# Performance work log

Hardware: AMD Instinct MI355X
Metric: run time of the kernel (lower is better)

The kernel has to match this reference:

```python
import jax, jax.numpy as jnp
import numpy as np

H = 128  # hidden_size
I = 28   # input_size
C = 10   # num_classes


def setup_inputs() -> dict:
    key = jax.random.key(0)
    ks = jax.random.split(key, 11)
    s = 1.0 / np.sqrt(H)  # torch nn.RNN init scale
    return {
        "x": jax.random.normal(ks[0], (8192, 28, I), dtype=jnp.float32),
        "W_ih0": jax.random.uniform(ks[1], (H, I), jnp.float32, -s, s),
        "W_hh0": jax.random.uniform(ks[2], (H, H), jnp.float32, -s, s),
        "b_ih0": jax.random.uniform(ks[3], (H,), jnp.float32, -s, s),
        "b_hh0": jax.random.uniform(ks[4], (H,), jnp.float32, -s, s),
        "W_ih1": jax.random.uniform(ks[5], (H, H), jnp.float32, -s, s),
        "W_hh1": jax.random.uniform(ks[6], (H, H), jnp.float32, -s, s),
        "b_ih1": jax.random.uniform(ks[7], (H,), jnp.float32, -s, s),
        "b_hh1": jax.random.uniform(ks[8], (H,), jnp.float32, -s, s),
        "fc_w": jax.random.uniform(ks[9], (C, H), jnp.float32, -s, s),
        "fc_b": jax.random.uniform(ks[10], (C,), jnp.float32, -s, s),
    }


def _rnn_layer_full(x, W_ih, b_ih, W_hh, b_hh):
    # x: [B, T, D] -> full output sequence [B, T, H]
    B = x.shape[0]
    h0 = jnp.zeros((B, H), x.dtype)
    xw = jnp.einsum('btd,hd->bth', x, W_ih) + b_ih  # precompute input GEMM

    def step(h, xw_t):
        h = jnp.tanh(xw_t + h @ W_hh.T + b_hh)
        return h, h

    _, ys = jax.lax.scan(step, h0, jnp.swapaxes(xw, 0, 1))  # [T, B, H]
    return jnp.swapaxes(ys, 0, 1)


def _rnn_layer_last(x, W_ih, b_ih, W_hh, b_hh):
    # only the final hidden state is needed downstream
    B = x.shape[0]
    h0 = jnp.zeros((B, H), x.dtype)
    xw = jnp.einsum('btd,hd->bth', x, W_ih) + b_ih

    def step(h, xw_t):
        h = jnp.tanh(xw_t + h @ W_hh.T + b_hh)
        return h, None

    h_last, _ = jax.lax.scan(step, h0, jnp.swapaxes(xw, 0, 1))
    return h_last


def reference(x, W_ih0, W_hh0, b_ih0, b_hh0, W_ih1, W_hh1, b_ih1, b_hh1, fc_w, fc_b):
    out0 = _rnn_layer_full(x, W_ih0, b_ih0, W_hh0, b_hh0)   # [B, T, H]
    h_last = _rnn_layer_last(out0, W_ih1, b_ih1, W_hh1, b_hh1)  # [B, H] == out[:, -1, :]
    return h_last @ fc_w.T + fc_b  # [B, C]
```

## Files before the change

kernel.cpp:

```cpp
#include <hip/hip_runtime.h>
#include <cmath>

#define HSZ 128
#define ISZ 28
#define TSZ 28
#define CSZ 10
#define BT  16
#define NT  256
#define HP  136

typedef _Float16 half_t;
typedef _Float16 v8h __attribute__((ext_vector_type(8)));
typedef float v4f __attribute__((ext_vector_type(4)));

__device__ __forceinline__ float fast_tanh(float x) {
    x = fminf(fmaxf(x, -15.f), 15.f);
    float e = __expf(2.f * x);
    return (e - 1.f) * __builtin_amdgcn_rcpf(e + 1.f);
}

__global__ __launch_bounds__(NT, 2)
void rnn_mfma(const float* __restrict__ x,
              const float* __restrict__ W_ih0, const float* __restrict__ W_hh0,
              const float* __restrict__ b_ih0, const float* __restrict__ b_hh0,
              const float* __restrict__ W_ih1, const float* __restrict__ W_hh1,
              const float* __restrict__ b_ih1, const float* __restrict__ b_hh1,
              const float* __restrict__ fc_w, const float* __restrict__ fc_b,
              float* __restrict__ out)
{
    __shared__ half_t h0s[2][BT][HP];
    __shared__ half_t h1s[2][BT][HP];
    __shared__ half_t xss[2][BT][32];

    const int tid  = threadIdx.x;
    const int wave = tid >> 6;
    const int lane = tid & 63;
    const int ln   = lane & 15;
    const int quad = lane >> 4;
    const int kq   = quad * 8;
    const int b0   = blockIdx.x * BT;

    v8h bWx[2];
    v8h bW0[2][4];
    v8h bW1i[2][4];
    v8h bW1h[2][4];
    float bias0v[2], bias1v[2];

#pragma unroll
    for (int nj = 0; nj < 2; ++nj) {
        const int c = (wave * 2 + nj) * 16 + ln;
        bias0v[nj] = b_ih0[c] + b_hh0[c];
        bias1v[nj] = b_ih1[c] + b_hh1[c];
#pragma unroll
        for (int j = 0; j < 8; ++j) {
            const int k = kq + j;
            bWx[nj][j] = (half_t)(k < ISZ ? W_ih0[c * ISZ + k] : 0.f);
        }
#pragma unroll
        for (int ks = 0; ks < 4; ++ks) {
            const float* p0 = W_hh0 + c * HSZ + ks * 32 + kq;
            const float* p1 = W_ih1 + c * HSZ + ks * 32 + kq;
            const float* p2 = W_hh1 + c * HSZ + ks * 32 + kq;
#pragma unroll
            for (int j = 0; j < 8; ++j) {
                bW0[nj][ks][j]  = (half_t)p0[j];
                bW1i[nj][ks][j] = (half_t)p1[j];
                bW1h[nj][ks][j] = (half_t)p2[j];
            }
        }
    }

    for (int idx = tid; idx < BT * HP; idx += NT) {
        (&h0s[0][0][0])[idx] = (half_t)0.f;
        (&h1s[0][0][0])[idx] = (half_t)0.f;
    }
    for (int idx = tid; idx < BT * 32; idx += NT) {
        const int m = idx >> 5, i = idx & 31;
        xss[0][m][i] = (half_t)(i < ISZ ? x[(size_t)(b0 + m) * (TSZ * ISZ) + i] : 0.f);
    }
    __syncthreads();

    int cA = 0, cB = 0;
    for (int t = 0; t < TSZ; ++t) {
        const int tb = t & 1;

        if (t + 1 < TSZ) {
            for (int idx = tid; idx < BT * 32; idx += NT) {
                const int m = idx >> 5, i = idx & 31;
                xss[tb ^ 1][m][i] =
                    (half_t)(i < ISZ ? x[(size_t)(b0 + m) * (TSZ * ISZ) + (t + 1) * ISZ + i]
                                     : 0.f);
            }
        }

        v4f acc[2];
#pragma unroll
        for (int nj = 0; nj < 2; ++nj)
            acc[nj] = (v4f){bias0v[nj], bias0v[nj], bias0v[nj], bias0v[nj]};
        {
            const v8h ax = *(const v8h*)&xss[tb][ln][kq];
#pragma unroll
            for (int nj = 0; nj < 2; ++nj)
                acc[nj] = __builtin_amdgcn_mfma_f32_16x16x32_f16(ax, bWx[nj], acc[nj], 0, 0, 0);
        }
#pragma unroll
        for (int ks = 0; ks < 4; ++ks) {
            const v8h ah = *(const v8h*)&h0s[cA][ln][ks * 32 + kq];
#pragma unroll
            for (int nj = 0; nj < 2; ++nj)
                acc[nj] = __builtin_amdgcn_mfma_f32_16x16x32_f16(ah, bW0[nj][ks], acc[nj], 0, 0, 0);
        }
#pragma unroll
        for (int nj = 0; nj < 2; ++nj) {
            const int c = (wave * 2 + nj) * 16 + ln;
#pragma unroll
            for (int r = 0; r < 4; ++r)
                h0s[cA ^ 1][quad * 4 + r][c] = (half_t)fast_tanh(acc[nj][r]);
        }
        __syncthreads();

#pragma unroll
        for (int nj = 0; nj < 2; ++nj)
            acc[nj] = (v4f){bias1v[nj], bias1v[nj], bias1v[nj], bias1v[nj]};
#pragma unroll
        for (int ks = 0; ks < 4; ++ks) {
            const v8h a0 = *(const v8h*)&h0s[cA ^ 1][ln][ks * 32 + kq];
#pragma unroll
            for (int nj = 0; nj < 2; ++nj)
                acc[nj] = __builtin_amdgcn_mfma_f32_16x16x32_f16(a0, bW1i[nj][ks], acc[nj], 0, 0, 0);
            const v8h a1 = *(const v8h*)&h1s[cB][ln][ks * 32 + kq];
#pragma unroll
            for (int nj = 0; nj < 2; ++nj)
                acc[nj] = __builtin_amdgcn_mfma_f32_16x16x32_f16(a1, bW1h[nj][ks], acc[nj], 0, 0, 0);
        }
#pragma unroll
        for (int nj = 0; nj < 2; ++nj) {
            const int c = (wave * 2 + nj) * 16 + ln;
#pragma unroll
            for (int r = 0; r < 4; ++r)
                h1s[cB ^ 1][quad * 4 + r][c] = (half_t)fast_tanh(acc[nj][r]);
        }
        __syncthreads();
        cA ^= 1; cB ^= 1;
    }

    for (int idx = tid; idx < BT * CSZ; idx += NT) {
        const int m = idx / CSZ, cc = idx - m * CSZ;
        float s = fc_b[cc];
#pragma unroll 4
        for (int k = 0; k < HSZ; ++k)
            s += (float)h1s[cB][m][k] * fc_w[cc * HSZ + k];
        out[(b0 + m) * CSZ + cc] = s;
    }
}

extern "C" void kernel_launch(void* const* d_in, const int* in_sizes, int n_in,
                              void* d_out, int out_size, void* d_ws, size_t ws_size,
                              hipStream_t stream) {
    const float* x     = (const float*)d_in[0];
    const float* W_ih0 = (const float*)d_in[1];
    const float* W_hh0 = (const float*)d_in[2];
    const float* b_ih0 = (const float*)d_in[3];
    const float* b_hh0 = (const float*)d_in[4];
    const float* W_ih1 = (const float*)d_in[5];
    const float* W_hh1 = (const float*)d_in[6];
    const float* b_ih1 = (const float*)d_in[7];
    const float* b_hh1 = (const float*)d_in[8];
    const float* fc_w  = (const float*)d_in[9];
    const float* fc_b  = (const float*)d_in[10];
    float* out = (float*)d_out;

    const int B = in_sizes[0] / (TSZ * ISZ);
    dim3 grid(B / BT), block(NT);
    rnn_mfma<<<grid, block, 0, stream>>>(x, W_ih0, W_hh0, b_ih0, b_hh0,
                                         W_ih1, W_hh1, b_ih1, b_hh1,
                                         fc_w, fc_b, out);
}
```

Measured before the change: 148.0 us.

## Skew layer-1 one step behind layer-0 to merge both recurrences per sync

Layer 1 now runs one timestep behind layer 0, so each iteration computes layer-0 step t+1 and layer-1 step t from the same loaded hidden states, with one barrier per step instead of two. The MFMA operands are swapped so weights are the A operand and hidden states the B operand, which lets tanh outputs be stored as packed 4-half vectors. The change also simplifies tanh by dropping the clamp, vectorizes the weight loads and the final FC, and adds a prologue and epilogue step. The cost is more live registers and a slightly more complex schedule; removing the clamp relies on exp overflow behaving well.

```diff
diff --git a/kernel.cpp b/kernel.cpp
--- a/kernel.cpp
+++ b/kernel.cpp
@@ -1,5 +1,4 @@
 #include <hip/hip_runtime.h>
-#include <cmath>
 
 #define HSZ 128
 #define ISZ 28
@@ -8,29 +7,30 @@
 #define BT  16
 #define NT  256
 #define HP  136
+#define XP  40
 
 typedef _Float16 half_t;
 typedef _Float16 v8h __attribute__((ext_vector_type(8)));
+typedef _Float16 v4h __attribute__((ext_vector_type(4)));
 typedef float v4f __attribute__((ext_vector_type(4)));
 
 __device__ __forceinline__ float fast_tanh(float x) {
-    x = fminf(fmaxf(x, -15.f), 15.f);
     float e = __expf(2.f * x);
-    return (e - 1.f) * __builtin_amdgcn_rcpf(e + 1.f);
+    return 1.f - 2.f * __builtin_amdgcn_rcpf(e + 1.f);
 }
 
 __global__ __launch_bounds__(NT, 2)
-void rnn_mfma(const float* __restrict__ x,
-              const float* __restrict__ W_ih0, const float* __restrict__ W_hh0,
-              const float* __restrict__ b_ih0, const float* __restrict__ b_hh0,
-              const float* __restrict__ W_ih1, const float* __restrict__ W_hh1,
-              const float* __restrict__ b_ih1, const float* __restrict__ b_hh1,
-              const float* __restrict__ fc_w, const float* __restrict__ fc_b,
-              float* __restrict__ out)
+void rnn_mfma2(const float* __restrict__ x,
+               const float* __restrict__ W_ih0, const float* __restrict__ W_hh0,
+               const float* __restrict__ b_ih0, const float* __restrict__ b_hh0,
+               const float* __restrict__ W_ih1, const float* __restrict__ W_hh1,
+               const float* __restrict__ b_ih1, const float* __restrict__ b_hh1,
+               const float* __restrict__ fc_w, const float* __restrict__ fc_b,
+               float* __restrict__ out)
 {
-    __shared__ half_t h0s[2][BT][HP];
-    __shared__ half_t h1s[2][BT][HP];
-    __shared__ half_t xss[2][BT][32];
+    __shared__ half_t h0s[2][BT * HP];
+    __shared__ half_t h1s[2][BT * HP];
+    __shared__ half_t xss[2][BT * XP];
 
     const int tid  = threadIdx.x;
     const int wave = tid >> 6;
@@ -40,116 +40,162 @@
     const int kq   = quad * 8;
     const int b0   = blockIdx.x * BT;
 
-    v8h bWx[2];
-    v8h bW0[2][4];
-    v8h bW1i[2][4];
-    v8h bW1h[2][4];
-    float bias0v[2], bias1v[2];
-
-#pragma unroll
-    for (int nj = 0; nj < 2; ++nj) {
-        const int c = (wave * 2 + nj) * 16 + ln;
-        bias0v[nj] = b_ih0[c] + b_hh0[c];
-        bias1v[nj] = b_ih1[c] + b_hh1[c];
+    v8h aWx[2];
+    v8h aW0[2][4];
+    v8h aW1i[2][4];
+    v8h aW1h[2][4];
+    v4f bias0[2], bias1[2];
+
+#pragma unroll
+    for (int nt = 0; nt < 2; ++nt) {
+        const int base = (wave * 2 + nt) * 16;
+        const int row  = base + ln;
+#pragma unroll
+        for (int r = 0; r < 4; ++r) {
+            const int c = base + quad * 4 + r;
+            bias0[nt][r] = b_ih0[c] + b_hh0[c];
+            bias1[nt][r] = b_ih1[c] + b_hh1[c];
+        }
 #pragma unroll
         for (int j = 0; j < 8; ++j) {
             const int k = kq + j;
-            bWx[nj][j] = (half_t)(k < ISZ ? W_ih0[c * ISZ + k] : 0.f);
-        }
-#pragma unroll
-        for (int ks = 0; ks < 4; ++ks) {
-            const float* p0 = W_hh0 + c * HSZ + ks * 32 + kq;
-            const float* p1 = W_ih1 + c * HSZ + ks * 32 + kq;
-            const float* p2 = W_hh1 + c * HSZ + ks * 32 + kq;
-#pragma unroll
-            for (int j = 0; j < 8; ++j) {
-                bW0[nj][ks][j]  = (half_t)p0[j];
-                bW1i[nj][ks][j] = (half_t)p1[j];
-                bW1h[nj][ks][j] = (half_t)p2[j];
+            aWx[nt][j] = (half_t)(k < ISZ ? W_ih0[row * ISZ + k] : 0.f);
+        }
+#pragma unroll
+        for (int ks = 0; ks < 4; ++ks) {
+            const float4* p0 = (const float4*)(W_hh0 + row * HSZ + ks * 32 + kq);
+            const float4* p1 = (const float4*)(W_ih1 + row * HSZ + ks * 32 + kq);
+            const float4* p2 = (const float4*)(W_hh1 + row * HSZ + ks * 32 + kq);
+            float4 a = p0[0], b = p0[1];
+            aW0[nt][ks] = (v8h){(half_t)a.x, (half_t)a.y, (half_t)a.z, (half_t)a.w,
+                                (half_t)b.x, (half_t)b.y, (half_t)b.z, (half_t)b.w};
+            a = p1[0]; b = p1[1];
+            aW1i[nt][ks] = (v8h){(half_t)a.x, (half_t)a.y, (half_t)a.z, (half_t)a.w,
+                                 (half_t)b.x, (half_t)b.y, (half_t)b.z, (half_t)b.w};
+            a = p2[0]; b = p2[1];
+            aW1h[nt][ks] = (v8h){(half_t)a.x, (half_t)a.y, (half_t)a.z, (half_t)a.w,
+                                 (half_t)b.x, (half_t)b.y, (half_t)b.z, (half_t)b.w};
+        }
+    }
+
+    for (int idx = tid; idx < BT * XP; idx += NT) {
+        xss[0][idx] = (half_t)0.f;
+        xss[1][idx] = (half_t)0.f;
+    }
+    for (int idx = tid; idx < BT * HP; idx += NT)
+        h1s[0][idx] = (half_t)0.f;
+    __syncthreads();
+    for (int idx = tid; idx < BT * ISZ; idx += NT) {
+        const int m = idx / ISZ, i = idx - m * ISZ;
+        const float* xr = x + (size_t)(b0 + m) * (TSZ * ISZ);
+        xss[0][m * XP + i] = (half_t)xr[i];
+        xss[1][m * XP + i] = (half_t)(ISZ + i < 2 * ISZ ? xr[ISZ + i] : 0.f);
+    }
+    __syncthreads();
+
+    {
+        const v8h bx = *(const v8h*)&xss[0][ln * XP + kq];
+        v4f a0[2] = {bias0[0], bias0[1]};
+#pragma unroll
+        for (int nt = 0; nt < 2; ++nt)
+            a0[nt] = __builtin_amdgcn_mfma_f32_16x16x32_f16(aWx[nt], bx, a0[nt], 0, 0, 0);
+#pragma unroll
+        for (int nt = 0; nt < 2; ++nt) {
+            const int base = (wave * 2 + nt) * 16;
+            v4h p = {(half_t)fast_tanh(a0[nt][0]), (half_t)fast_tanh(a0[nt][1]),
+                     (half_t)fast_tanh(a0[nt][2]), (half_t)fast_tanh(a0[nt][3])};
+            *(v4h*)&h0s[0][ln * HP + base + quad * 4] = p;
+        }
+    }
+    __syncthreads();
+
+    for (int t = 0; t < TSZ - 1; ++t) {
+        const int pr = t & 1;
+
+        if (t < TSZ - 2) {
+            for (int idx = tid; idx < BT * ISZ; idx += NT) {
+                const int m = idx / ISZ, i = idx - m * ISZ;
+                xss[pr][m * XP + i] =
+                    (half_t)x[(size_t)(b0 + m) * (TSZ * ISZ) + (t + 2) * ISZ + i];
             }
         }
-    }
-
-    for (int idx = tid; idx < BT * HP; idx += NT) {
-        (&h0s[0][0][0])[idx] = (half_t)0.f;
-        (&h1s[0][0][0])[idx] = (half_t)0.f;
-    }
-    for (int idx = tid; idx < BT * 32; idx += NT) {
-        const int m = idx >> 5, i = idx & 31;
-        xss[0][m][i] = (half_t)(i < ISZ ? x[(size_t)(b0 + m) * (TSZ * ISZ) + i] : 0.f);
-    }
-    __syncthreads();
-
-    int cA = 0, cB = 0;
-    for (int t = 0; t < TSZ; ++t) {
-        const int tb = t & 1;
-
-        if (t + 1 < TSZ) {
-            for (int idx = tid; idx < BT * 32; idx += NT) {
-                const int m = idx >> 5, i = idx & 31;
-                xss[tb ^ 1][m][i] =
-                    (half_t)(i < ISZ ? x[(size_t)(b0 + m) * (TSZ * ISZ) + (t + 1) * ISZ + i]
-                                     : 0.f);
+
+        v8h bh0[4], bh1[4];
+#pragma unroll
+        for (int ks = 0; ks < 4; ++ks) {
+            bh0[ks] = *(const v8h*)&h0s[pr][ln * HP + ks * 32 + kq];
+            bh1[ks] = *(const v8h*)&h1s[pr][ln * HP + ks * 32 + kq];
+        }
+        const v8h bx = *(const v8h*)&xss[pr ^ 1][ln * XP + kq];
+
+        v4f a1[2] = {bias1[0], bias1[1]};
+        v4f a0[2] = {bias0[0], bias0[1]};
+#pragma unroll
+        for (int nt = 0; nt < 2; ++nt)
+            a0[nt] = __builtin_amdgcn_mfma_f32_16x16x32_f16(aWx[nt], bx, a0[nt], 0, 0, 0);
+#pragma unroll
+        for (int ks = 0; ks < 4; ++ks) {
+#pragma unroll
+            for (int nt = 0; nt < 2; ++nt) {
+                a1[nt] = __builtin_amdgcn_mfma_f32_16x16x32_f16(aW1i[nt][ks], bh0[ks], a1[nt], 0, 0, 0);
+                a1[nt] = __builtin_amdgcn_mfma_f32_16x16x32_f16(aW1h[nt][ks], bh1[ks], a1[nt], 0, 0, 0);
+                a0[nt] = __builtin_amdgcn_mfma_f32_16x16x32_f16(aW0[nt][ks], bh0[ks], a0[nt], 0, 0, 0);
             }
         }
 
-        v4f acc[2];
-#pragma unroll
-        for (int nj = 0; nj < 2; ++nj)
-            acc[nj] = (v4f){bias0v[nj], bias0v[nj], bias0v[nj], bias0v[nj]};
-        {
-            const v8h ax = *(const v8h*)&xss[tb][ln][kq];
-#pragma unroll
-            for (int nj = 0; nj < 2; ++nj)
-                acc[nj] = __builtin_amdgcn_mfma_f32_16x16x32_f16(ax, bWx[nj], acc[nj], 0, 0, 0);
-        }
-#pragma unroll
-        for (int ks = 0; ks < 4; ++ks) {
-            const v8h ah = *(const v8h*)&h0s[cA][ln][ks * 32 + kq];
-#pragma unroll
-            for (int nj = 0; nj < 2; ++nj)
-                acc[nj] = __builtin_amdgcn_mfma_f32_16x16x32_f16(ah, bW0[nj][ks], acc[nj], 0, 0, 0);
-        }
-#pragma unroll
-        for (int nj = 0; nj < 2; ++nj) {
-            const int c = (wave * 2 + nj) * 16 + ln;
-#pragma unroll
-            for (int r = 0; r < 4; ++r)
-                h0s[cA ^ 1][quad * 4 + r][c] = (half_t)fast_tanh(acc[nj][r]);
+#pragma unroll
+        for (int nt = 0; nt < 2; ++nt) {
+            const int base = (wave * 2 + nt) * 16;
+            v4h p1 = {(half_t)fast_tanh(a1[nt][0]), (half_t)fast_tanh(a1[nt][1]),
+                      (half_t)fast_tanh(a1[nt][2]), (half_t)fast_tanh(a1[nt][3])};
+            *(v4h*)&h1s[pr ^ 1][ln * HP + base + quad * 4] = p1;
+            v4h p0 = {(half_t)fast_tanh(a0[nt][0]), (half_t)fast_tanh(a0[nt][1]),
+                      (half_t)fast_tanh(a0[nt][2]), (half_t)fast_tanh(a0[nt][3])};
+            *(v4h*)&h0s[pr ^ 1][ln * HP + base + quad * 4] = p0;
         }
         __syncthreads();
-
-#pragma unroll
-        for (int nj = 0; nj < 2; ++nj)
-            acc[nj] = (v4f){bias1v[nj], bias1v[nj], bias1v[nj], bias1v[nj]};
-#pragma unroll
-        for (int ks = 0; ks < 4; ++ks) {
-            const v8h a0 = *(const v8h*)&h0s[cA ^ 1][ln][ks * 32 + kq];
-#pragma unroll
-            for (int nj = 0; nj < 2; ++nj)
-                acc[nj] = __builtin_amdgcn_mfma_f32_16x16x32_f16(a0, bW1i[nj][ks], acc[nj], 0, 0, 0);
-            const v8h a1 = *(const v8h*)&h1s[cB][ln][ks * 32 + kq];
-#pragma unroll
-            for (int nj = 0; nj < 2; ++nj)
-                acc[nj] = __builtin_amdgcn_mfma_f32_16x16x32_f16(a1, bW1h[nj][ks], acc[nj], 0, 0, 0);
-        }
-#pragma unroll
-        for (int nj = 0; nj < 2; ++nj) {
-            const int c = (wave * 2 + nj) * 16 + ln;
-#pragma unroll
-            for (int r = 0; r < 4; ++r)
-                h1s[cB ^ 1][quad * 4 + r][c] = (half_t)fast_tanh(acc[nj][r]);
+    }
+
+    {
+        const int pr = (TSZ - 1) & 1;
+        v8h bh0[4], bh1[4];
+#pragma unroll
+        for (int ks = 0; ks < 4; ++ks) {
+            bh0[ks] = *(const v8h*)&h0s[pr][ln * HP + ks * 32 + kq];
+            bh1[ks] = *(const v8h*)&h1s[pr][ln * HP + ks * 32 + kq];
+        }
+        v4f a1[2] = {bias1[0], bias1[1]};
+#pragma unroll
+        for (int ks = 0; ks < 4; ++ks) {
+#pragma unroll
+            for (int nt = 0; nt < 2; ++nt) {
+                a1[nt] = __builtin_amdgcn_mfma_f32_16x16x32_f16(aW1i[nt][ks], bh0[ks], a1[nt], 0, 0, 0);
+                a1[nt] = __builtin_amdgcn_mfma_f32_16x16x32_f16(aW1h[nt][ks], bh1[ks], a1[nt], 0, 0, 0);
+            }
+        }
+#pragma unroll
+        for (int nt = 0; nt < 2; ++nt) {
+            const int base = (wave * 2 + nt) * 16;
+            v4h p1 = {(half_t)fast_tanh(a1[nt][0]), (half_t)fast_tanh(a1[nt][1]),
+                      (half_t)fast_tanh(a1[nt][2]), (half_t)fast_tanh(a1[nt][3])};
+            *(v4h*)&h1s[pr ^ 1][ln * HP + base + quad * 4] = p1;
         }
         __syncthreads();
-        cA ^= 1; cB ^= 1;
-    }
-
-    for (int idx = tid; idx < BT * CSZ; idx += NT) {
-        const int m = idx / CSZ, cc = idx - m * CSZ;
+    }
+
+    if (tid < BT * CSZ) {
+        const int m = tid / CSZ, cc = tid - m * CSZ;
         float s = fc_b[cc];
-#pragma unroll 4
-        for (int k = 0; k < HSZ; ++k)
-            s += (float)h1s[cB][m][k] * fc_w[cc * HSZ + k];
+#pragma unroll
+        for (int k8 = 0; k8 < HSZ / 8; ++k8) {
+            const v8h hv = *(const v8h*)&h1s[0][m * HP + k8 * 8];
+            const float4 w0 = *(const float4*)(fc_w + cc * HSZ + k8 * 8);
+            const float4 w1 = *(const float4*)(fc_w + cc * HSZ + k8 * 8 + 4);
+            s += (float)hv[0] * w0.x + (float)hv[1] * w0.y +
+                 (float)hv[2] * w0.z + (float)hv[3] * w0.w +
+                 (float)hv[4] * w1.x + (float)hv[5] * w1.y +
+                 (float)hv[6] * w1.z + (float)hv[7] * w1.w;
+        }
         out[(b0 + m) * CSZ + cc] = s;
     }
 }
@@ -172,7 +218,7 @@
 
     const int B = in_sizes[0] / (TSZ * ISZ);
     dim3 grid(B / BT), block(NT);
-    rnn_mfma<<<grid, block, 0, stream>>>(x, W_ih0, W_hh0, b_ih0, b_hh0,
-                                         W_ih1, W_hh1, b_ih1, b_hh1,
-                                         fc_w, fc_b, out);
+    rnn_mfma2<<<grid, block, 0, stream>>>(x, W_ih0, W_hh0, b_ih0, b_hh0,
+                                          W_ih1, W_hh1, b_ih1, b_hh1,
+                                          fc_w, fc_b, out);
 }
```

After: 140.2 us. 5.2% less time.
